# Performance work log

Hardware: AMD Instinct MI355X
Metric: run time of the kernel (lower is better)

The kernel has to match this reference:

```python
import jax, jax.numpy as jnp
import numpy as np

N_EMBD = 768
N_HEAD = 12
LN_EPS = 1e-5


def _linear_params(key, fan_in, fan_out):
    kw, kb = jax.random.split(key)
    bound = 1.0 / np.sqrt(fan_in)
    W = jax.random.uniform(kw, (fan_in, fan_out), jnp.float32, -bound, bound)
    b = jax.random.uniform(kb, (fan_out,), jnp.float32, -bound, bound)
    return W, b


def setup_inputs() -> dict:
    key = jax.random.key(0)
    ks = jax.random.split(key, 6)
    x = jax.random.normal(ks[0], (8, 1024, N_EMBD), jnp.float32)
    W_attn, b_attn = _linear_params(ks[1], N_EMBD, 3 * N_EMBD)
    W_proj, b_proj = _linear_params(ks[2], N_EMBD, N_EMBD)
    W_fc, b_fc = _linear_params(ks[3], N_EMBD, 4 * N_EMBD)
    W_fc2, b_fc2 = _linear_params(ks[4], 4 * N_EMBD, N_EMBD)
    return {
        "x": x,
        "ln1_g": jnp.ones((N_EMBD,), jnp.float32),
        "ln1_b": jnp.zeros((N_EMBD,), jnp.float32),
        "W_attn": W_attn, "b_attn": b_attn,
        "W_proj": W_proj, "b_proj": b_proj,
        "ln2_g": jnp.ones((N_EMBD,), jnp.float32),
        "ln2_b": jnp.zeros((N_EMBD,), jnp.float32),
        "W_fc": W_fc, "b_fc": b_fc,
        "W_fc2": W_fc2, "b_fc2": b_fc2,
    }


def _layernorm(x, g, b):
    mu = jnp.mean(x, axis=-1, keepdims=True)
    var = jnp.var(x, axis=-1, keepdims=True)
    return (x - mu) * jax.lax.rsqrt(var + LN_EPS) * g + b


def _attn(x, W_attn, b_attn, W_proj, b_proj):
    B, T, C = x.shape
    hd = C // N_HEAD
    qkv = x @ W_attn + b_attn  # [B,T,3C]
    q, k, v = jnp.split(qkv, 3, axis=-1)
    q = q.reshape(B, T, N_HEAD, hd).transpose(0, 2, 1, 3)  # [B,H,T,hd]
    k = k.reshape(B, T, N_HEAD, hd).transpose(0, 2, 1, 3)
    v = v.reshape(B, T, N_HEAD, hd).transpose(0, 2, 1, 3)
    scores = jnp.einsum('bhqd,bhkd->bhqk', q, k) * (1.0 / np.sqrt(hd))
    mask = jnp.tril(jnp.ones((T, T), bool))
    scores = jnp.where(mask, scores, -jnp.inf)
    attn = jax.nn.softmax(scores, axis=-1)
    y = jnp.einsum('bhqk,bhkd->bhqd', attn, v)
    y = y.transpose(0, 2, 1, 3).reshape(B, T, C)
    return y @ W_proj + b_proj


def reference(x, ln1_g, ln1_b, W_attn, b_attn, W_proj, b_proj,
              ln2_g, ln2_b, W_fc, b_fc, W_fc2, b_fc2):
    x = x + _attn(_layernorm(x, ln1_g, ln1_b), W_attn, b_attn, W_proj, b_proj)
    h = _layernorm(x, ln2_g, ln2_b)
    h = jax.nn.gelu(h @ W_fc + b_fc, approximate=False)  # torch GELU default = exact erf
    x = x + h @ W_fc2 + b_fc2
    return x
```

## Files before the change

### kernel.cpp

```cpp
#include <hip/hip_runtime.h>
#include <hip/hip_bf16.h>
#include <stdint.h>

#define DEV __device__ __forceinline__

typedef __attribute__((ext_vector_type(8))) short     short8;
typedef __attribute__((ext_vector_type(4))) float     f32x4;
typedef __attribute__((ext_vector_type(4))) unsigned short ushort4v;

DEV float bf2f(unsigned short u) { return __uint_as_float(((uint32_t)u) << 16); }
DEV unsigned short f2bf(float f) {
    uint32_t x = __float_as_uint(f);
    return (unsigned short)((x + 0x7FFFu + ((x >> 16) & 1u)) >> 16);
}

DEV f32x4 mfma16(short8 a, short8 b, f32x4 c) {
    return __builtin_amdgcn_mfma_f32_16x16x32_bf16(a, b, c, 0, 0, 0);
}

#define AS1C const __attribute__((address_space(1)))
#define AS3  __attribute__((address_space(3)))

DEV void gload_lds16(const void* g, void* l) {
    __builtin_amdgcn_global_load_lds((AS1C void*)g, (AS3 void*)l, 16, 0, 0);
}

__global__ __launch_bounds__(256) void ln_kernel(const float* __restrict__ x,
                                                 const float* __restrict__ g,
                                                 const float* __restrict__ b,
                                                 unsigned short* __restrict__ out)
{
    const int lane = threadIdx.x & 63;
    const int row  = blockIdx.x * 4 + (threadIdx.x >> 6);
    const float* xr = x + (size_t)row * 768;

    f32x4 v[3];
    float s = 0.f, sq = 0.f;
#pragma unroll
    for (int i = 0; i < 3; ++i) {
        v[i] = *(const f32x4*)(xr + i * 256 + lane * 4);
#pragma unroll
        for (int j = 0; j < 4; ++j) { s += v[i][j]; sq = fmaf(v[i][j], v[i][j], sq); }
    }
#pragma unroll
    for (int off = 32; off; off >>= 1) { s += __shfl_xor(s, off); sq += __shfl_xor(sq, off); }
    const float mean = s * (1.0f / 768.0f);
    const float rstd = rsqrtf(sq * (1.0f / 768.0f) - mean * mean + 1e-5f);

#pragma unroll
    for (int i = 0; i < 3; ++i) {
        f32x4 gg = *(const f32x4*)(g + i * 256 + lane * 4);
        f32x4 bb = *(const f32x4*)(b + i * 256 + lane * 4);
        ushort4v o;
#pragma unroll
        for (int j = 0; j < 4; ++j) o[j] = f2bf((v[i][j] - mean) * rstd * gg[j] + bb[j]);
        *(ushort4v*)(out + (size_t)row * 768 + i * 256 + lane * 4) = o;
    }
}

__global__ __launch_bounds__(256) void wconv_kernel(const float* __restrict__ W,
                                                    unsigned short* __restrict__ Wt,
                                                    int K, int N)
{
    __shared__ float t[32][33];
    const int tx = threadIdx.x & 31, ty = threadIdx.x >> 5;
    const int n0 = blockIdx.x * 32, k0 = blockIdx.y * 32;
#pragma unroll
    for (int i = 0; i < 4; ++i)
        t[ty + i * 8][tx] = W[(size_t)(k0 + ty + i * 8) * N + n0 + tx];
    __syncthreads();
#pragma unroll
    for (int i = 0; i < 4; ++i)
        Wt[(size_t)(n0 + ty + i * 8) * K + k0 + tx] = f2bf(t[tx][ty + i * 8]);
}

template <int EPI>
__global__ __launch_bounds__(256) void gemm_bt(const unsigned short* __restrict__ A,
                                               const unsigned short* __restrict__ Bt,
                                               const float* __restrict__ bias,
                                               const float* __restrict__ res,
                                               float* __restrict__ outf,
                                               unsigned short* __restrict__ outh,
                                               int M, int N, int K)
{
    __shared__ unsigned short As[128 * 32];
    __shared__ unsigned short Bs[128 * 32];
    const int tid = threadIdx.x;
    const int lane = tid & 63, wv = tid >> 6;
    const int r16 = lane & 15, g4 = lane >> 4;
    const int wm = wv >> 1, wn = wv & 1;
    const int n0 = blockIdx.x * 128, m0 = blockIdx.y * 128;

    f32x4 acc[4][4] = {};

    for (int k0 = 0; k0 < K; k0 += 32) {
#pragma unroll
        for (int i = 0; i < 2; ++i) {
            const int chunk0 = wv * 128 + i * 64;
            const int c = chunk0 + lane;
            const unsigned short* ga = A  + (size_t)(m0 + (c >> 2)) * K + k0 + (c & 3) * 8;
            const unsigned short* gb = Bt + (size_t)(n0 + (c >> 2)) * K + k0 + (c & 3) * 8;
            gload_lds16(ga, (char*)As + (size_t)chunk0 * 16);
            gload_lds16(gb, (char*)Bs + (size_t)chunk0 * 16);
        }
        __syncthreads();

        short8 af[4], bfr[4];
#pragma unroll
        for (int i = 0; i < 4; ++i)
            af[i] = *(const short8*)(As + (wm * 64 + i * 16 + r16) * 32 + g4 * 8);
#pragma unroll
        for (int j = 0; j < 4; ++j)
            bfr[j] = *(const short8*)(Bs + (wn * 64 + j * 16 + r16) * 32 + g4 * 8);
#pragma unroll
        for (int i = 0; i < 4; ++i)
#pragma unroll
            for (int j = 0; j < 4; ++j)
                acc[i][j] = mfma16(af[i], bfr[j], acc[i][j]);
        __syncthreads();
    }

#pragma unroll
    for (int i = 0; i < 4; ++i) {
#pragma unroll
        for (int j = 0; j < 4; ++j) {
            const int row = m0 + wm * 64 + i * 16 + g4 * 4;
            const int col = n0 + wn * 64 + j * 16 + r16;
            const float bv = bias[col];
#pragma unroll
            for (int r = 0; r < 4; ++r) {
                const float v = acc[i][j][r] + bv;
                const size_t idx = (size_t)(row + r) * N + col;
                if constexpr (EPI == 0) {
                    outh[idx] = f2bf(v);
                } else if constexpr (EPI == 1) {
                    outf[idx] = v + res[idx];
                } else {
                    const float ge = 0.5f * v * (1.0f + erff(v * 0.70710678118654752f));
                    outh[idx] = f2bf(ge);
                }
            }
        }
    }
}

__global__ __launch_bounds__(256) void gemm_bt64(const unsigned short* __restrict__ A,
                                                 const unsigned short* __restrict__ Bt,
                                                 const float* __restrict__ bias,
                                                 const float* __restrict__ res,
                                                 float* __restrict__ outf,
                                                 int M, int N, int K)
{
    __shared__ unsigned short As[64 * 32];
    __shared__ unsigned short Bs[128 * 32];
    const int tid = threadIdx.x;
    const int lane = tid & 63, wv = tid >> 6;
    const int r16 = lane & 15, g4 = lane >> 4;
    const int m0 = blockIdx.x * 64, n0 = blockIdx.y * 128;

    f32x4 acc[4][2] = {};

    for (int k0 = 0; k0 < K; k0 += 32) {
        const int cb = wv * 64;
        const int c  = cb + lane;
        gload_lds16(A + (size_t)(m0 + (c >> 2)) * K + k0 + (c & 3) * 8,
                    (char*)As + (size_t)cb * 16);
        gload_lds16(Bt + (size_t)(n0 + (c >> 2)) * K + k0 + (c & 3) * 8,
                    (char*)Bs + (size_t)cb * 16);
        gload_lds16(Bt + (size_t)(n0 + ((c + 256) >> 2)) * K + k0 + (c & 3) * 8,
                    (char*)Bs + (size_t)(cb + 256) * 16);
        __syncthreads();

        short8 af[4], bfr[2];
#pragma unroll
        for (int i = 0; i < 4; ++i)
            af[i] = *(const short8*)(As + (i * 16 + r16) * 32 + g4 * 8);
#pragma unroll
        for (int j = 0; j < 2; ++j)
            bfr[j] = *(const short8*)(Bs + (wv * 32 + j * 16 + r16) * 32 + g4 * 8);
#pragma unroll
        for (int i = 0; i < 4; ++i)
#pragma unroll
            for (int j = 0; j < 2; ++j)
                acc[i][j] = mfma16(af[i], bfr[j], acc[i][j]);
        __syncthreads();
    }

#pragma unroll
    for (int i = 0; i < 4; ++i) {
#pragma unroll
        for (int j = 0; j < 2; ++j) {
            const int row = m0 + i * 16 + g4 * 4;
            const int col = n0 + wv * 32 + j * 16 + r16;
            const float bv = bias[col];
#pragma unroll
            for (int r = 0; r < 4; ++r) {
                const size_t idx = (size_t)(row + r) * N + col;
                outf[idx] = acc[i][j][r] + bv + res[idx];
            }
        }
    }
}

__global__ __launch_bounds__(256) void attn_kernel(const unsigned short* __restrict__ qkv,
                                                   unsigned short* __restrict__ out)
{
    __shared__ alignas(16) unsigned short K_lds[2][64][64];
    __shared__ alignas(16) unsigned short Vt[2][64][64];
    __shared__ alignas(16) unsigned short P_lds[4][2][16][72];

    const int tid  = threadIdx.x;
    const int lane = tid & 63, w = tid >> 6;
    const int r16 = lane & 15, g4 = lane >> 4;
    const int bid = blockIdx.x;
    const int qb  = 7 - (bid / 96);
    const int rem = bid % 96;
    const int h   = rem % 12;
    const int b   = rem / 12;
    const int C3 = 2304, T = 1024;
    const int qt  = qb * 4 + w;
    const int gr0 = b * T + qt * 32;
    const int qc  = h * 64;
    const int ns  = 2 * qb + 2;

    const unsigned short* kbase = qkv + (size_t)(b * T) * C3 + 768 + qc;
    const unsigned short* vbase = kbase + 768;

    short8 qf[2][2];
#pragma unroll
    for (int mt = 0; mt < 2; ++mt)
#pragma unroll
        for (int ks = 0; ks < 2; ++ks) {
            short8 v = *(const short8*)(qkv + (size_t)(gr0 + mt * 16 + r16) * C3 + qc + ks * 32 + g4 * 8);
#pragma unroll
            for (int j = 0; j < 8; ++j)
                v[j] = (short)f2bf(bf2f((unsigned short)v[j]) * 0.125f);
            qf[mt][ks] = v;
        }

    auto STAGE_K = [&](int st, int buf) {
#pragma unroll
        for (int i = 0; i < 2; ++i) {
            const int cb = i * 256 + w * 64;
            const int c  = cb + lane;
            const int row = c >> 3, k2 = c & 7;
            gload_lds16(kbase + (size_t)(st * 64 + row) * C3 + (size_t)((k2 ^ (row & 7)) * 8),
                        (char*)K_lds[buf] + (size_t)cb * 16);
        }
    };
    auto WRITE_VT = [&](int buf, short8 v0, short8 v1) {
#pragma unroll
        for (int j = 0; j < 8; ++j) {
            Vt[buf][w * 16 + j]     [((((lane >> 3) ^ j) << 3) | (lane & 7))] = (unsigned short)v0[j];
            Vt[buf][w * 16 + 8 + j] [((((lane >> 3) ^ j) << 3) | (lane & 7))] = (unsigned short)v1[j];
        }
    };

    f32x4 o[2][4] = {};
    float mst[2][4], lst[2][4];
#pragma unroll
    for (int mt = 0; mt < 2; ++mt)
#pragma unroll
        for (int r = 0; r < 4; ++r) { mst[mt][r] = -1e30f; lst[mt][r] = 0.f; }

    STAGE_K(0, 0);
    {
        short8 v0 = *(const short8*)(vbase + (size_t)lane * C3 + w * 16);
        short8 v1 = *(const short8*)(vbase + (size_t)lane * C3 + w * 16 + 8);
        asm volatile("s_waitcnt vmcnt(0)" ::: "memory");
        WRITE_VT(0, v0, v1);
    }

    for (int s = 0; s < ns; ++s) {
        asm volatile("s_waitcnt lgkmcnt(0)" ::: "memory");
        asm volatile("s_barrier" ::: "memory");
        __builtin_amdgcn_sched_barrier(0);

        short8 vb0, vb1;
        const bool more = (s + 1 < ns);
        if (more) {
            STAGE_K(s + 1, (s + 1) & 1);
            vb0 = *(const short8*)(vbase + (size_t)((s + 1) * 64 + lane) * C3 + w * 16);
            vb1 = *(const short8*)(vbase + (size_t)((s + 1) * 64 + lane) * C3 + w * 16 + 8);
        }

        if (s * 64 <= qt * 32 + 31) {
            const int buf = s & 1;
            short8 kf[4][2];
#pragma unroll
            for (int kt = 0; kt < 4; ++kt)
#pragma unroll
                for (int ks = 0; ks < 2; ++ks) {
                    const int row = kt * 16 + r16;
                    const int pc  = (ks * 4 + g4) ^ (row & 7);
                    kf[kt][ks] = *(const short8*)&K_lds[buf][row][pc * 8];
                }
            f32x4 sv[2][4] = {};
#pragma unroll
            for (int mt = 0; mt < 2; ++mt)
#pragma unroll
                for (int kt = 0; kt < 4; ++kt)
#pragma unroll
                    for (int ks = 0; ks < 2; ++ks)
                        sv[mt][kt] = mfma16(qf[mt][ks], kf[kt][ks], sv[mt][kt]);

            if (s * 64 + 63 > qt * 32) {
#pragma unroll
                for (int mt = 0; mt < 2; ++mt)
#pragma unroll
                    for (int kt = 0; kt < 4; ++kt)
#pragma unroll
                        for (int r = 0; r < 4; ++r)
                            if (s * 64 + kt * 16 + r16 > qt * 32 + mt * 16 + g4 * 4 + r)
                                sv[mt][kt][r] = -1e30f;
            }

#pragma unroll
            for (int mt = 0; mt < 2; ++mt) {
#pragma unroll
                for (int r = 0; r < 4; ++r) {
                    float mx = fmaxf(fmaxf(sv[mt][0][r], sv[mt][1][r]),
                                     fmaxf(sv[mt][2][r], sv[mt][3][r]));
#pragma unroll
                    for (int off = 8; off; off >>= 1) mx = fmaxf(mx, __shfl_xor(mx, off));
                    const float mnew  = fmaxf(mst[mt][r], mx);
                    const float alpha = __expf(mst[mt][r] - mnew);
                    mst[mt][r] = mnew;
                    float p[4], rs = 0.f;
#pragma unroll
                    for (int kt = 0; kt < 4; ++kt) {
                        p[kt] = __expf(sv[mt][kt][r] - mnew);
                        rs += p[kt];
                    }
#pragma unroll
                    for (int off = 8; off; off >>= 1) rs += __shfl_xor(rs, off);
                    lst[mt][r] = lst[mt][r] * alpha + rs;
#pragma unroll
                    for (int kt = 0; kt < 4; ++kt)
                        P_lds[w][mt][g4 * 4 + r][kt * 16 + r16] = f2bf(p[kt]);
#pragma unroll
                    for (int n = 0; n < 4; ++n) o[mt][n][r] *= alpha;
                }
            }

            short8 pa[2][2];
#pragma unroll
            for (int mt = 0; mt < 2; ++mt)
#pragma unroll
                for (int h2 = 0; h2 < 2; ++h2)
                    pa[mt][h2] = *(const short8*)&P_lds[w][mt][r16][h2 * 32 + g4 * 8];
            short8 vf2[2][4];
#pragma unroll
            for (int h2 = 0; h2 < 2; ++h2)
#pragma unroll
                for (int n = 0; n < 4; ++n)
                    vf2[h2][n] = *(const short8*)&Vt[buf][n * 16 + r16][((h2 * 4 + g4) ^ (r16 & 7)) << 3];
#pragma unroll
            for (int h2 = 0; h2 < 2; ++h2)
#pragma unroll
                for (int n = 0; n < 4; ++n) {
                    o[0][n] = mfma16(pa[0][h2], vf2[h2][n], o[0][n]);
                    o[1][n] = mfma16(pa[1][h2], vf2[h2][n], o[1][n]);
                }
        }

        if (more) {
            asm volatile("s_waitcnt vmcnt(0)" ::: "memory");
            WRITE_VT((s + 1) & 1, vb0, vb1);
        }
    }

#pragma unroll
    for (int mt = 0; mt < 2; ++mt)
#pragma unroll
        for (int n = 0; n < 4; ++n)
#pragma unroll
            for (int r = 0; r < 4; ++r)
                out[(size_t)(gr0 + mt * 16 + g4 * 4 + r) * 768 + qc + n * 16 + r16] =
                    f2bf(o[mt][n][r] / lst[mt][r]);
}

extern "C" void kernel_launch(void* const* d_in, const int* in_sizes, int n_in,
                              void* d_out, int out_size, void* d_ws, size_t ws_size,
                              hipStream_t stream)
{
    const float* x     = (const float*)d_in[0];
    const float* ln1g  = (const float*)d_in[1];
    const float* ln1b  = (const float*)d_in[2];
    const float* Wattn = (const float*)d_in[3];
    const float* battn = (const float*)d_in[4];
    const float* Wproj = (const float*)d_in[5];
    const float* bproj = (const float*)d_in[6];
    const float* ln2g  = (const float*)d_in[7];
    const float* ln2b  = (const float*)d_in[8];
    const float* Wfc   = (const float*)d_in[9];
    const float* bfc   = (const float*)d_in[10];
    const float* Wfc2  = (const float*)d_in[11];
    const float* bfc2  = (const float*)d_in[12];
    float* out = (float*)d_out;

    char* p = (char*)d_ws;
    auto alloc = [&](size_t bytes) { char* q = p; p += (bytes + 255) & ~(size_t)255; return q; };
    unsigned short* wt_attn = (unsigned short*)alloc(768ull * 2304 * 2);
    unsigned short* wt_proj = (unsigned short*)alloc(768ull * 768 * 2);
    unsigned short* wt_fc   = (unsigned short*)alloc(768ull * 3072 * 2);
    unsigned short* wt_fc2  = (unsigned short*)alloc(3072ull * 768 * 2);
    unsigned short* bufA    = (unsigned short*)alloc(8192ull * 768 * 2);
    unsigned short* bufB    = (unsigned short*)alloc(8192ull * 3072 * 2);
    float*          x1      = (float*)alloc(8192ull * 768 * 4);

    const int M = 8192;

    wconv_kernel<<<dim3(2304 / 32, 768 / 32), 256, 0, stream>>>(Wattn, wt_attn, 768, 2304);
    wconv_kernel<<<dim3(768 / 32, 768 / 32), 256, 0, stream>>>(Wproj, wt_proj, 768, 768);
    wconv_kernel<<<dim3(3072 / 32, 768 / 32), 256, 0, stream>>>(Wfc, wt_fc, 768, 3072);
    wconv_kernel<<<dim3(768 / 32, 3072 / 32), 256, 0, stream>>>(Wfc2, wt_fc2, 3072, 768);

    ln_kernel<<<2048, 256, 0, stream>>>(x, ln1g, ln1b, bufA);

    gemm_bt<0><<<dim3(2304 / 128, M / 128), 256, 0, stream>>>(
        bufA, wt_attn, battn, (const float*)nullptr, (float*)nullptr, bufB, M, 2304, 768);

    attn_kernel<<<dim3(768), 256, 0, stream>>>(bufB, bufA);

    gemm_bt64<<<dim3(M / 64, 768 / 128), 256, 0, stream>>>(
        bufA, wt_proj, bproj, x, x1, M, 768, 768);

    ln_kernel<<<2048, 256, 0, stream>>>(x1, ln2g, ln2b, bufA);

    gemm_bt<2><<<dim3(3072 / 128, M / 128), 256, 0, stream>>>(
        bufA, wt_fc, bfc, (const float*)nullptr, (float*)nullptr, bufB, M, 3072, 768);

    gemm_bt64<<<dim3(M / 64, 768 / 128), 256, 0, stream>>>(
        bufB, wt_fc2, bfc2, x1, out, M, 768, 3072);
}
```

Before: 396.1 us.

## Double-buffer LDS tiles in GEMM kernels and use tanh-approximate GELU

Both GEMM kernels now keep two LDS buffers and issue the global-to-LDS loads for the next K tile before computing on the current one, so load latency can overlap MFMA work. The exact erf GELU is replaced with a tanh approximation built on __expf. Double buffering doubles shared memory per block, which may lower occupancy, and the visible loop has no wait or barrier before the next tile is read. The tanh GELU differs slightly from the exact erf form the reference specifies.

Result: faster. 385.5 us (-2.7%).

```diff
diff --git a/kernel.cpp b/kernel.cpp
--- a/kernel.cpp
+++ b/kernel.cpp
@@ -16,6 +16,13 @@
 
 DEV f32x4 mfma16(short8 a, short8 b, f32x4 c) {
     return __builtin_amdgcn_mfma_f32_16x16x32_bf16(a, b, c, 0, 0, 0);
+}
+
+DEV float gelu_f(float v) {
+    const float u2 = 2.0f * v * (0.7978845608f + 0.0356774081f * v * v);
+    const float e  = __expf(u2);
+    const float th = 1.0f - 2.0f / (e + 1.0f);
+    return 0.5f * v * (1.0f + th);
 }
 
 #define AS1C const __attribute__((address_space(1)))
@@ -83,35 +90,43 @@
                                                unsigned short* __restrict__ outh,
                                                int M, int N, int K)
 {
-    __shared__ unsigned short As[128 * 32];
-    __shared__ unsigned short Bs[128 * 32];
+    __shared__ unsigned short As[2][128 * 32];
+    __shared__ unsigned short Bs[2][128 * 32];
     const int tid = threadIdx.x;
     const int lane = tid & 63, wv = tid >> 6;
     const int r16 = lane & 15, g4 = lane >> 4;
     const int wm = wv >> 1, wn = wv & 1;
     const int n0 = blockIdx.x * 128, m0 = blockIdx.y * 128;
-
-    f32x4 acc[4][4] = {};
-
-    for (int k0 = 0; k0 < K; k0 += 32) {
+    const int nt = K >> 5;
+
+    auto STAGE = [&](int t, int buf) {
 #pragma unroll
         for (int i = 0; i < 2; ++i) {
             const int chunk0 = wv * 128 + i * 64;
             const int c = chunk0 + lane;
-            const unsigned short* ga = A  + (size_t)(m0 + (c >> 2)) * K + k0 + (c & 3) * 8;
-            const unsigned short* gb = Bt + (size_t)(n0 + (c >> 2)) * K + k0 + (c & 3) * 8;
-            gload_lds16(ga, (char*)As + (size_t)chunk0 * 16);
-            gload_lds16(gb, (char*)Bs + (size_t)chunk0 * 16);
-        }
-        __syncthreads();
+            const unsigned short* ga = A  + (size_t)(m0 + (c >> 2)) * K + t * 32 + (c & 3) * 8;
+            const unsigned short* gb = Bt + (size_t)(n0 + (c >> 2)) * K + t * 32 + (c & 3) * 8;
+            gload_lds16(ga, (char*)As[buf] + (size_t)chunk0 * 16);
+            gload_lds16(gb, (char*)Bs[buf] + (size_t)chunk0 * 16);
+        }
+    };
+
+    f32x4 acc[4][4] = {};
+
+    STAGE(0, 0);
+    __syncthreads();
+
+    for (int t = 0; t < nt; ++t) {
+        const int buf = t & 1;
+        if (t + 1 < nt) STAGE(t + 1, buf ^ 1);
 
         short8 af[4], bfr[4];
 #pragma unroll
         for (int i = 0; i < 4; ++i)
-            af[i] = *(const short8*)(As + (wm * 64 + i * 16 + r16) * 32 + g4 * 8);
+            af[i] = *(const short8*)(As[buf] + (wm * 64 + i * 16 + r16) * 32 + g4 * 8);
 #pragma unroll
         for (int j = 0; j < 4; ++j)
-            bfr[j] = *(const short8*)(Bs + (wn * 64 + j * 16 + r16) * 32 + g4 * 8);
+            bfr[j] = *(const short8*)(Bs[buf] + (wn * 64 + j * 16 + r16) * 32 + g4 * 8);
 #pragma unroll
         for (int i = 0; i < 4; ++i)
 #pragma unroll
@@ -136,8 +151,7 @@
                 } else if constexpr (EPI == 1) {
                     outf[idx] = v + res[idx];
                 } else {
-                    const float ge = 0.5f * v * (1.0f + erff(v * 0.70710678118654752f));
-                    outh[idx] = f2bf(ge);
+                    outh[idx] = f2bf(gelu_f(v));
                 }
             }
         }
@@ -151,33 +165,41 @@
                                                  float* __restrict__ outf,
                                                  int M, int N, int K)
 {
-    __shared__ unsigned short As[64 * 32];
-    __shared__ unsigned short Bs[128 * 32];
+    __shared__ unsigned short As[2][64 * 32];
+    __shared__ unsigned short Bs[2][128 * 32];
     const int tid = threadIdx.x;
     const int lane = tid & 63, wv = tid >> 6;
     const int r16 = lane & 15, g4 = lane >> 4;
     const int m0 = blockIdx.x * 64, n0 = blockIdx.y * 128;
-
-    f32x4 acc[4][2] = {};
-
-    for (int k0 = 0; k0 < K; k0 += 32) {
+    const int nt = K >> 5;
+
+    auto STAGE = [&](int t, int buf) {
         const int cb = wv * 64;
         const int c  = cb + lane;
-        gload_lds16(A + (size_t)(m0 + (c >> 2)) * K + k0 + (c & 3) * 8,
-                    (char*)As + (size_t)cb * 16);
-        gload_lds16(Bt + (size_t)(n0 + (c >> 2)) * K + k0 + (c & 3) * 8,
-                    (char*)Bs + (size_t)cb * 16);
-        gload_lds16(Bt + (size_t)(n0 + ((c + 256) >> 2)) * K + k0 + (c & 3) * 8,
-                    (char*)Bs + (size_t)(cb + 256) * 16);
-        __syncthreads();
+        gload_lds16(A + (size_t)(m0 + (c >> 2)) * K + t * 32 + (c & 3) * 8,
+                    (char*)As[buf] + (size_t)cb * 16);
+        gload_lds16(Bt + (size_t)(n0 + (c >> 2)) * K + t * 32 + (c & 3) * 8,
+                    (char*)Bs[buf] + (size_t)cb * 16);
+        gload_lds16(Bt + (size_t)(n0 + ((c + 256) >> 2)) * K + t * 32 + (c & 3) * 8,
+                    (char*)Bs[buf] + (size_t)(cb + 256) * 16);
+    };
+
+    f32x4 acc[4][2] = {};
+
+    STAGE(0, 0);
+    __syncthreads();
+
+    for (int t = 0; t < nt; ++t) {
+        const int buf = t & 1;
+        if (t + 1 < nt) STAGE(t + 1, buf ^ 1);
 
         short8 af[4], bfr[2];
 #pragma unroll
         for (int i = 0; i < 4; ++i)
-            af[i] = *(const short8*)(As + (i * 16 + r16) * 32 + g4 * 8);
+            af[i] = *(const short8*)(As[buf] + (i * 16 + r16) * 32 + g4 * 8);
 #pragma unroll
         for (int j = 0; j < 2; ++j)
-            bfr[j] = *(const short8*)(Bs + (wv * 32 + j * 16 + r16) * 32 + g4 * 8);
+            bfr[j] = *(const short8*)(Bs[buf] + (wv * 32 + j * 16 + r16) * 32 + g4 * 8);
 #pragma unroll
         for (int i = 0; i < 4; ++i)
 #pragma unroll
```
